# Kernel optimization log

Measured on AMD Instinct MI355X. Metric: run time of the kernel, lower is better.

Reference implementation:

```python
import jax, jax.numpy as jnp
import numpy as np

WIN = 8          # window size
SHIFT = 4        # shift size
NH = 6           # num heads
HD = 32          # head dim
DIM = NH * HD    # 192
SCALE = HD ** (-0.5)
B, H, W = 4, 256, 256

def _rel_index():
    coords = np.stack(np.meshgrid(np.arange(WIN), np.arange(WIN), indexing='ij'))  # (2,w,w)
    cf = coords.reshape(2, -1)                       # (2, w*w)
    rel = (cf[:, :, None] - cf[:, None, :]).transpose(1, 2, 0)  # (w*w, w*w, 2)
    rel[..., 0] += WIN - 1
    rel[..., 1] += WIN - 1
    rel[..., 0] *= 2 * WIN - 1
    return rel.sum(-1)                               # (w*w, w*w) int

REL_IDX = _rel_index()

def _shift_mask(h, w):
    # same construction as get_shift_mask (static shapes -> plain numpy)
    m = np.zeros((h, w))
    cnt = 0
    for hs in (slice(0, -WIN), slice(-WIN, -SHIFT), slice(-SHIFT, None)):
        for ws in (slice(0, -WIN), slice(-WIN, -SHIFT), slice(-SHIFT, None)):
            m[hs, ws] = cnt
            cnt += 1
    # mask_window_partition -> (nW, win_seq)
    m = m.reshape(h // WIN, WIN, w // WIN, WIN).transpose(0, 2, 1, 3).reshape(-1, WIN * WIN)
    am = m[:, None, :] - m[:, :, None]               # unsqueeze(1) - unsqueeze(2)
    return np.where(am != 0, -100.0, 0.0).astype(np.float32)  # (nW, ws^2, ws^2)

SHIFT_MASK = _shift_mask(H, W)

def setup_inputs() -> dict:
    key = jax.random.key(0)
    k1, k2 = jax.random.split(key)
    x = jax.random.normal(k1, (B, 3 * DIM, H, W), dtype=jnp.float32)
    rpb_table = jax.random.normal(k2, ((2 * WIN - 1) ** 2, NH), dtype=jnp.float32) * 0.02
    return {"x": x, "rpb_table": rpb_table}

def reference(x, rpb_table):
    b, _, h, w = x.shape
    nwh, nww = h // WIN, w // WIN
    nw = nwh * nww
    ws2 = WIN * WIN
    if SHIFT > 0:
        x = jnp.roll(x, shift=(-SHIFT, -SHIFT), axis=(2, 3))
    # winP: (B, 3*C, H, W) -> (3, B*nW, NH, ws^2, HD)
    qkv = x.reshape(b, 3, NH, HD, nwh, WIN, nww, WIN)
    qkv = qkv.transpose(1, 0, 4, 6, 2, 5, 7, 3).reshape(3, b * nw, NH, ws2, HD)
    q, k, v = qkv[0], qkv[1], qkv[2]
    att = jnp.einsum('wnqd,wnkd->wnqk', q, k) * SCALE   # (B*nW, NH, ws^2, ws^2)
    rpb = rpb_table[REL_IDX.reshape(-1)].reshape(ws2, ws2, NH).transpose(2, 0, 1)
    att = att + rpb[None]
    if SHIFT > 0:
        mask = jnp.asarray(SHIFT_MASK)                  # (nW, ws^2, ws^2)
        att = att.reshape(b, nw, NH, ws2, ws2) + mask[None, :, None]
        att = att.reshape(b * nw, NH, ws2, ws2)
    att = jax.nn.softmax(att, axis=-1)
    out = jnp.einsum('wnqk,wnkd->wnqd', att, v)         # (B*nW, NH, ws^2, HD)
    # winR: back to (B, NH*HD, H, W)
    out = out.reshape(b, nwh, nww, NH, WIN, WIN, HD)
    out = out.transpose(0, 3, 6, 1, 4, 2, 5).reshape(b, NH * HD, h, w)
    if SHIFT > 0:
        out = jnp.roll(out, shift=(SHIFT, SHIFT), axis=(2, 3))
    return out
```

## Files before the change

### kernel.cpp

```cpp
#include <hip/hip_runtime.h>

#define NH 6
#define HD 32
#define WIN 8
#define NWH 32
#define HWSZ 65536
#define SCALE 0.17677669529663687f

__global__ __launch_bounds__(64, 2)
void swin_attn_kernel(const float* __restrict__ x,
                      const float* __restrict__ rpb,
                      float* __restrict__ out) {
  __shared__ float Kt[HD * 64];
  __shared__ float Vt[HD * 64];
  __shared__ float rpb_s[228];

  const int raw = (int)blockIdx.x;
  const int lid = (raw & 7) * 3072 + (raw >> 3);
  const int ww = lid & 31;
  int t = lid >> 5;
  const int nh = t % NH;
  t /= NH;
  const int wh = t & 31;
  const int b  = t >> 5;

  const int lane = threadIdx.x;

  {
    const int dly = lane >> 4;
    const int s0  = (lane & 15) << 2;
    const int iy  = s0 >> 3;
    const int ix0 = s0 & 7;
    const int sh  = (wh * WIN + 4 + iy) & 255;
    const int sw  = (ww * WIN + 4 + ix0) & 255;
    const size_t base = (size_t)(b * 576 + nh * HD + dly) * HWSZ + (size_t)sh * 256 + sw;
    const float* gk = x + base + (size_t)192 * HWSZ;
    const float* gv = x + base + (size_t)384 * HWSZ;
#pragma unroll
    for (int i = 0; i < 8; ++i) {
      __builtin_amdgcn_global_load_lds(
          (const __attribute__((address_space(1))) void*)(gk + (size_t)i * 4 * HWSZ),
          (__attribute__((address_space(3))) void*)(&Kt[i * 256]), 16, 0, 0);
      __builtin_amdgcn_global_load_lds(
          (const __attribute__((address_space(1))) void*)(gv + (size_t)i * 4 * HWSZ),
          (__attribute__((address_space(3))) void*)(&Vt[i * 256]), 16, 0, 0);
    }
  }

  for (int r = lane; r < 225; r += 64) rpb_s[r] = rpb[r * NH + nh];

  const int qy = lane >> 3, qx = lane & 7;
  const int sh = (wh * WIN + 4 + qy) & 255;
  const int sw = (ww * WIN + 4 + qx) & 255;
  const float* qbase = x + (size_t)(b * 576 + nh * HD) * HWSZ + (size_t)sh * 256 + sw;
  float Qr[HD];
#pragma unroll
  for (int d = 0; d < HD; ++d) Qr[d] = qbase[(size_t)d * HWSZ];

  __syncthreads();

  float att[64];
#pragma unroll
  for (int k = 0; k < 64; ++k) att[k] = 0.f;
#pragma unroll 2
  for (int d = 0; d < HD; ++d) {
    const float qd = Qr[d];
    const float4* kp = (const float4*)&Kt[d * 64];
#pragma unroll
    for (int j = 0; j < 16; ++j) {
      const float4 kv = kp[j];
      att[4*j+0] = fmaf(qd, kv.x, att[4*j+0]);
      att[4*j+1] = fmaf(qd, kv.y, att[4*j+1]);
      att[4*j+2] = fmaf(qd, kv.z, att[4*j+2]);
      att[4*j+3] = fmaf(qd, kv.w, att[4*j+3]);
    }
  }

  const bool eh = (wh == NWH - 1), ew = (ww == NWH - 1);
  const int rq = (eh ? 1 + (qy >> 2) : 0) * 3 + (ew ? 1 + (qx >> 2) : 0);
  const int qoff = (qy + 7) * 15 + (qx + 7);
  float m = -1e30f;
#pragma unroll
  for (int k = 0; k < 64; ++k) {
    const int ky = k >> 3, kx = k & 7;
    float a = fmaf(att[k], SCALE, rpb_s[qoff - (ky * 15 + kx)]);
    const int rk = (eh ? 1 + (ky >> 2) : 0) * 3 + (ew ? 1 + (kx >> 2) : 0);
    a += (rk == rq) ? 0.f : -100.f;
    att[k] = a;
    m = fmaxf(m, a);
  }

  float p0 = 0.f, p1 = 0.f, p2 = 0.f, p3 = 0.f;
#pragma unroll
  for (int k = 0; k < 64; k += 4) {
    att[k+0] = __expf(att[k+0] - m); p0 += att[k+0];
    att[k+1] = __expf(att[k+1] - m); p1 += att[k+1];
    att[k+2] = __expf(att[k+2] - m); p2 += att[k+2];
    att[k+3] = __expf(att[k+3] - m); p3 += att[k+3];
  }
  const float rsum = 1.f / (p0 + p1 + p2 + p3);

  float* obase = out + (size_t)(b * 192 + nh * HD) * HWSZ + (size_t)sh * 256 + sw;
#pragma unroll 2
  for (int dv = 0; dv < HD; ++dv) {
    const float4* vp = (const float4*)&Vt[dv * 64];
    float a0 = 0.f, a1 = 0.f, a2 = 0.f, a3 = 0.f;
#pragma unroll
    for (int j = 0; j < 16; ++j) {
      const float4 vv = vp[j];
      a0 = fmaf(att[4*j+0], vv.x, a0);
      a1 = fmaf(att[4*j+1], vv.y, a1);
      a2 = fmaf(att[4*j+2], vv.z, a2);
      a3 = fmaf(att[4*j+3], vv.w, a3);
    }
    obase[(size_t)dv * HWSZ] = (a0 + a1 + a2 + a3) * rsum;
  }
}

extern "C" void kernel_launch(void* const* d_in, const int* in_sizes, int n_in,
                              void* d_out, int out_size, void* d_ws, size_t ws_size,
                              hipStream_t stream) {
  const float* x   = (const float*)d_in[0];
  const float* rpb = (const float*)d_in[1];
  float* out = (float*)d_out;
  dim3 grid(4 * 32 * 32 * NH);
  dim3 block(64);
  hipLaunchKernelGGL(swin_attn_kernel, grid, block, 0, stream, x, rpb, out);
}
```

Before: 1.108 ms.

## Compute window attention with bf16x3 split MFMA instead of scalar FMA

```diff
diff --git a/kernel.cpp b/kernel.cpp
--- a/kernel.cpp
+++ b/kernel.cpp
@@ -1,119 +1,204 @@
 #include <hip/hip_runtime.h>
 
 #define NH 6
-#define HD 32
-#define WIN 8
-#define NWH 32
 #define HWSZ 65536
 #define SCALE 0.17677669529663687f
 
+typedef __attribute__((ext_vector_type(8)))  short short8t;
+typedef __attribute__((ext_vector_type(16))) float f32x16;
+typedef __attribute__((ext_vector_type(4)))  unsigned int uint4t;
+
+__device__ __forceinline__ unsigned int pack2(float a, float b) {
+  return (__float_as_uint(a) >> 16) | (__float_as_uint(b) & 0xffff0000u);
+}
+__device__ __forceinline__ float btrunc_f(float a) {
+  return __uint_as_float(__float_as_uint(a) & 0xffff0000u);
+}
+__device__ __forceinline__ float resid(float a) { return a - btrunc_f(a); }
+
+__device__ __forceinline__ void split8(const float (&f)[8], short8t& h, short8t& l) {
+  uint4t hw, lw;
+#pragma unroll
+  for (int i = 0; i < 4; ++i) {
+    const float a = f[2*i], c = f[2*i+1];
+    hw[i] = pack2(a, c);
+    lw[i] = pack2(resid(a), resid(c));
+  }
+  h = __builtin_bit_cast(short8t, hw);
+  l = __builtin_bit_cast(short8t, lw);
+}
+
 __global__ __launch_bounds__(64, 2)
-void swin_attn_kernel(const float* __restrict__ x,
-                      const float* __restrict__ rpb,
-                      float* __restrict__ out) {
-  __shared__ float Kt[HD * 64];
-  __shared__ float Vt[HD * 64];
-  __shared__ float rpb_s[228];
+void swin_attn_mfma(const float* __restrict__ x,
+                    const float* __restrict__ rpb,
+                    float* __restrict__ out) {
+  __shared__ float Vt[2048];
+  __shared__ float rpb_s[232];
 
   const int raw = (int)blockIdx.x;
   const int lid = (raw & 7) * 3072 + (raw >> 3);
   const int ww = lid & 31;
   int t = lid >> 5;
-  const int nh = t % NH;
-  t /= NH;
+  const int nh = t % NH; t /= NH;
   const int wh = t & 31;
   const int b  = t >> 5;
 
-  const int lane = threadIdx.x;
+  const int lane = (int)threadIdx.x;
+  const int lo = lane & 31, hi = lane >> 5;
 
   {
     const int dly = lane >> 4;
-    const int s0  = (lane & 15) << 2;
-    const int iy  = s0 >> 3;
-    const int ix0 = s0 & 7;
-    const int sh  = (wh * WIN + 4 + iy) & 255;
-    const int sw  = (ww * WIN + 4 + ix0) & 255;
-    const size_t base = (size_t)(b * 576 + nh * HD + dly) * HWSZ + (size_t)sh * 256 + sw;
-    const float* gk = x + base + (size_t)192 * HWSZ;
-    const float* gv = x + base + (size_t)384 * HWSZ;
+    const int chp = (lane & 15) >> 1;
+    const int off0 = (lane & 1) * 4;
+    const int s0e = ((chp ^ dly) << 3) + off0;
+    const int s0o = ((chp ^ (4 + dly)) << 3) + off0;
+    const size_t cb = (size_t)(b * 576 + 384 + nh * 32 + dly) * HWSZ;
+    const float* gve = x + cb + (size_t)(((wh*8+4+(s0e>>3)) & 255) * 256 + ((ww*8+4+(s0e&7)) & 255));
+    const float* gvo = x + cb + (size_t)(((wh*8+4+(s0o>>3)) & 255) * 256 + ((ww*8+4+(s0o&7)) & 255));
 #pragma unroll
     for (int i = 0; i < 8; ++i) {
+      const float* src = (i & 1) ? gvo : gve;
       __builtin_amdgcn_global_load_lds(
-          (const __attribute__((address_space(1))) void*)(gk + (size_t)i * 4 * HWSZ),
-          (__attribute__((address_space(3))) void*)(&Kt[i * 256]), 16, 0, 0);
-      __builtin_amdgcn_global_load_lds(
-          (const __attribute__((address_space(1))) void*)(gv + (size_t)i * 4 * HWSZ),
+          (const __attribute__((address_space(1))) void*)(src + (size_t)i * 4 * HWSZ),
           (__attribute__((address_space(3))) void*)(&Vt[i * 256]), 16, 0, 0);
     }
   }
-
   for (int r = lane; r < 225; r += 64) rpb_s[r] = rpb[r * NH + nh];
 
-  const int qy = lane >> 3, qx = lane & 7;
-  const int sh = (wh * WIN + 4 + qy) & 255;
-  const int sw = (ww * WIN + 4 + qx) & 255;
-  const float* qbase = x + (size_t)(b * 576 + nh * HD) * HWSZ + (size_t)sh * 256 + sw;
-  float Qr[HD];
-#pragma unroll
-  for (int d = 0; d < HD; ++d) Qr[d] = qbase[(size_t)d * HWSZ];
+  const int iy = lo >> 3, ix = lo & 7;
+  const int sh0 = (wh*8 + 4 + iy) & 255;
+  const int sh1 = (wh*8 + 8 + iy) & 255;
+  const int sw  = (ww*8 + 4 + ix) & 255;
+  const size_t pix0 = (size_t)sh0 * 256 + sw;
+  const size_t pix1 = (size_t)sh1 * 256 + sw;
+  const size_t qcb = (size_t)(b * 576 + nh * 32) * HWSZ;
+  const size_t kcb = qcb + (size_t)192 * HWSZ;
+
+  short8t qh[2][2], ql[2][2], kh[2][2], kl[2][2];
+#pragma unroll
+  for (int ks = 0; ks < 2; ++ks) {
+#pragma unroll
+    for (int tt = 0; tt < 2; ++tt) {
+      const size_t pp = tt ? pix1 : pix0;
+      float f[8], g[8];
+#pragma unroll
+      for (int e = 0; e < 8; ++e) {
+        const size_t dof = (size_t)(ks*16 + hi*8 + e) * HWSZ;
+        f[e] = x[qcb + dof + pp];
+        g[e] = x[kcb + dof + pp];
+      }
+      split8(f, qh[ks][tt], ql[ks][tt]);
+      split8(g, kh[ks][tt], kl[ks][tt]);
+    }
+  }
+
+  f32x16 acc[2][2];
+#pragma unroll
+  for (int mt = 0; mt < 2; ++mt)
+#pragma unroll
+    for (int nt = 0; nt < 2; ++nt)
+#pragma unroll
+      for (int r = 0; r < 16; ++r) acc[mt][nt][r] = 0.f;
+
+#pragma unroll
+  for (int ks = 0; ks < 2; ++ks)
+#pragma unroll
+    for (int mt = 0; mt < 2; ++mt)
+#pragma unroll
+      for (int nt = 0; nt < 2; ++nt) {
+        acc[mt][nt] = __builtin_amdgcn_mfma_f32_32x32x16_bf16(kh[ks][mt], qh[ks][nt], acc[mt][nt], 0, 0, 0);
+        acc[mt][nt] = __builtin_amdgcn_mfma_f32_32x32x16_bf16(kh[ks][mt], ql[ks][nt], acc[mt][nt], 0, 0, 0);
+        acc[mt][nt] = __builtin_amdgcn_mfma_f32_32x32x16_bf16(kl[ks][mt], qh[ks][nt], acc[mt][nt], 0, 0, 0);
+      }
 
   __syncthreads();
 
-  float att[64];
-#pragma unroll
-  for (int k = 0; k < 64; ++k) att[k] = 0.f;
-#pragma unroll 2
-  for (int d = 0; d < HD; ++d) {
-    const float qd = Qr[d];
-    const float4* kp = (const float4*)&Kt[d * 64];
-#pragma unroll
-    for (int j = 0; j < 16; ++j) {
-      const float4 kv = kp[j];
-      att[4*j+0] = fmaf(qd, kv.x, att[4*j+0]);
-      att[4*j+1] = fmaf(qd, kv.y, att[4*j+1]);
-      att[4*j+2] = fmaf(qd, kv.z, att[4*j+2]);
-      att[4*j+3] = fmaf(qd, kv.w, att[4*j+3]);
-    }
-  }
-
-  const bool eh = (wh == NWH - 1), ew = (ww == NWH - 1);
-  const int rq = (eh ? 1 + (qy >> 2) : 0) * 3 + (ew ? 1 + (qx >> 2) : 0);
-  const int qoff = (qy + 7) * 15 + (qx + 7);
-  float m = -1e30f;
-#pragma unroll
-  for (int k = 0; k < 64; ++k) {
-    const int ky = k >> 3, kx = k & 7;
-    float a = fmaf(att[k], SCALE, rpb_s[qoff - (ky * 15 + kx)]);
-    const int rk = (eh ? 1 + (ky >> 2) : 0) * 3 + (ew ? 1 + (kx >> 2) : 0);
-    a += (rk == rq) ? 0.f : -100.f;
-    att[k] = a;
-    m = fmaxf(m, a);
-  }
-
-  float p0 = 0.f, p1 = 0.f, p2 = 0.f, p3 = 0.f;
-#pragma unroll
-  for (int k = 0; k < 64; k += 4) {
-    att[k+0] = __expf(att[k+0] - m); p0 += att[k+0];
-    att[k+1] = __expf(att[k+1] - m); p1 += att[k+1];
-    att[k+2] = __expf(att[k+2] - m); p2 += att[k+2];
-    att[k+3] = __expf(att[k+3] - m); p3 += att[k+3];
-  }
-  const float rsum = 1.f / (p0 + p1 + p2 + p3);
-
-  float* obase = out + (size_t)(b * 192 + nh * HD) * HWSZ + (size_t)sh * 256 + sw;
-#pragma unroll 2
-  for (int dv = 0; dv < HD; ++dv) {
-    const float4* vp = (const float4*)&Vt[dv * 64];
-    float a0 = 0.f, a1 = 0.f, a2 = 0.f, a3 = 0.f;
-#pragma unroll
-    for (int j = 0; j < 16; ++j) {
-      const float4 vv = vp[j];
-      a0 = fmaf(att[4*j+0], vv.x, a0);
-      a1 = fmaf(att[4*j+1], vv.y, a1);
-      a2 = fmaf(att[4*j+2], vv.z, a2);
-      a3 = fmaf(att[4*j+3], vv.w, a3);
-    }
-    obase[(size_t)dv * HWSZ] = (a0 + a1 + a2 + a3) * rsum;
+  const bool eh = (wh == 31), ew = (ww == 31);
+  float mrow[2] = {-1e30f, -1e30f};
+#pragma unroll
+  for (int nt = 0; nt < 2; ++nt) {
+    const int qyy = 4*nt + iy;
+    const int rq = (eh ? 1 + (qyy >> 2) : 0) * 3 + (ew ? 1 + (ix >> 2) : 0);
+    const int qoff = (qyy + 7) * 15 + (ix + 7);
+#pragma unroll
+    for (int mt = 0; mt < 2; ++mt)
+#pragma unroll
+      for (int r = 0; r < 16; ++r) {
+        const int ky = 4*mt + (r >> 2);
+        const int kx = 4*hi + (r & 3);
+        float a = fmaf(acc[mt][nt][r], SCALE, rpb_s[qoff - ky*15 - kx]);
+        const int rk = (eh ? 1 + (ky >> 2) : 0) * 3 + (ew ? 1 + (kx >> 2) : 0);
+        a += (rk == rq) ? 0.f : -100.f;
+        acc[mt][nt][r] = a;
+        mrow[nt] = fmaxf(mrow[nt], a);
+      }
+  }
+  mrow[0] = fmaxf(mrow[0], __shfl_xor(mrow[0], 32));
+  mrow[1] = fmaxf(mrow[1], __shfl_xor(mrow[1], 32));
+
+  float sum0 = 0.f, sum1 = 0.f;
+#pragma unroll
+  for (int mt = 0; mt < 2; ++mt)
+#pragma unroll
+    for (int r = 0; r < 16; ++r) {
+      const float p0 = __expf(acc[mt][0][r] - mrow[0]);
+      const float p1 = __expf(acc[mt][1][r] - mrow[1]);
+      acc[mt][0][r] = p0; sum0 += p0;
+      acc[mt][1][r] = p1; sum1 += p1;
+    }
+  sum0 += __shfl_xor(sum0, 32);
+  sum1 += __shfl_xor(sum1, 32);
+  const float rs0 = 1.f / sum0, rs1 = 1.f / sum1;
+
+  f32x16 oacc[2];
+#pragma unroll
+  for (int r = 0; r < 16; ++r) { oacc[0][r] = 0.f; oacc[1][r] = 0.f; }
+
+#pragma unroll
+  for (int ks2 = 0; ks2 < 4; ++ks2) {
+    const int mt = ks2 >> 1, bs = (ks2 & 1) * 8;
+    float vf[8];
+    {
+      const int chp = (2*ks2 + hi) ^ (lo & 7);
+      const float4 v0 = *(const float4*)&Vt[lo*64 + chp*8];
+      const float4 v1 = *(const float4*)&Vt[lo*64 + chp*8 + 4];
+      vf[0]=v0.x; vf[1]=v0.y; vf[2]=v0.z; vf[3]=v0.w;
+      vf[4]=v1.x; vf[5]=v1.y; vf[6]=v1.z; vf[7]=v1.w;
+    }
+    short8t vh, vl; split8(vf, vh, vl);
+#pragma unroll
+    for (int nt = 0; nt < 2; ++nt) {
+      const float a0 = acc[mt][nt][bs+0], a1 = acc[mt][nt][bs+1];
+      const float a2 = acc[mt][nt][bs+2], a3 = acc[mt][nt][bs+3];
+      const float b0 = acc[mt][nt][bs+4], b1 = acc[mt][nt][bs+5];
+      const float b2 = acc[mt][nt][bs+6], b3 = acc[mt][nt][bs+7];
+      const unsigned int Ah0 = pack2(a0, a1), Ah1 = pack2(a2, a3);
+      const unsigned int Bh0 = pack2(b0, b1), Bh1 = pack2(b2, b3);
+      const unsigned int Al0 = pack2(resid(a0), resid(a1)), Al1 = pack2(resid(a2), resid(a3));
+      const unsigned int Bl0 = pack2(resid(b0), resid(b1)), Bl1 = pack2(resid(b2), resid(b3));
+      const unsigned int xAh0 = __shfl_xor(Ah0, 32), xAh1 = __shfl_xor(Ah1, 32);
+      const unsigned int xBh0 = __shfl_xor(Bh0, 32), xBh1 = __shfl_xor(Bh1, 32);
+      const unsigned int xAl0 = __shfl_xor(Al0, 32), xAl1 = __shfl_xor(Al1, 32);
+      const unsigned int xBl0 = __shfl_xor(Bl0, 32), xBl1 = __shfl_xor(Bl1, 32);
+      uint4t wh4, wl4;
+      wh4[0] = hi ? xBh0 : Ah0;  wh4[1] = hi ? xBh1 : Ah1;
+      wh4[2] = hi ? Bh0 : xAh0;  wh4[3] = hi ? Bh1 : xAh1;
+      wl4[0] = hi ? xBl0 : Al0;  wl4[1] = hi ? xBl1 : Al1;
+      wl4[2] = hi ? Bl0 : xAl0;  wl4[3] = hi ? Bl1 : xAl1;
+      const short8t pbh = __builtin_bit_cast(short8t, wh4);
+      const short8t pbl = __builtin_bit_cast(short8t, wl4);
+      oacc[nt] = __builtin_amdgcn_mfma_f32_32x32x16_bf16(vh, pbh, oacc[nt], 0, 0, 0);
+      oacc[nt] = __builtin_amdgcn_mfma_f32_32x32x16_bf16(vh, pbl, oacc[nt], 0, 0, 0);
+      oacc[nt] = __builtin_amdgcn_mfma_f32_32x32x16_bf16(vl, pbh, oacc[nt], 0, 0, 0);
+    }
+  }
+
+  const size_t ocb = (size_t)(b * 192 + nh * 32) * HWSZ;
+#pragma unroll
+  for (int r = 0; r < 16; ++r) {
+    const int d = 4*hi + (r & 3) + 8*(r >> 2);
+    out[ocb + (size_t)d * HWSZ + pix0] = oacc[0][r] * rs0;
+    out[ocb + (size_t)d * HWSZ + pix1] = oacc[1][r] * rs1;
   }
 }
 
@@ -125,5 +210,5 @@
   float* out = (float*)d_out;
   dim3 grid(4 * 32 * 32 * NH);
   dim3 block(64);
-  hipLaunchKernelGGL(swin_attn_kernel, grid, block, 0, stream, x, rpb, out);
-}
+  hipLaunchKernelGGL(swin_attn_mfma, grid, block, 0, stream, x, rpb, out);
+}
```

After: 1.006 ms. 1.1x faster.
